# Kernel tuning notes

Measured on AMD Instinct MI355X. Metric: run time of the kernel, lower is better.

The kernel has to match this reference:

```python
import jax, jax.numpy as jnp
import numpy as np

D_K = 64

def setup_inputs() -> dict:
    key = jax.random.key(0)
    kx, kq, kk, kv = jax.random.split(key, 4)
    B, T, D = 4, 2048, 1024
    s = 1.0 / np.sqrt(D)
    return {
        "x": jax.random.normal(kx, (B, T, D), dtype=jnp.float32),
        "Wq": jax.random.normal(kq, (D, D_K), dtype=jnp.float32) * s,
        "Wk": jax.random.normal(kk, (D, D_K), dtype=jnp.float32) * s,
        "Wv": jax.random.normal(kv, (D, D_K), dtype=jnp.float32) * s,
    }

def reference(x, Wq, Wk, Wv):
    # x: [B, T, D]; Wq/Wk/Wv: [D, d_k]
    Q = x @ Wq  # [B, T, d_k]
    K = x @ Wk
    V = x @ Wv
    scale = 1.0 / jnp.sqrt(jnp.asarray(Q.shape[-1], Q.dtype))
    scores = jnp.einsum('btd,bsd->bts', Q, K) * scale  # [B, T, T]
    T = scores.shape[-1]
    causal = jnp.tril(jnp.ones((T, T), dtype=bool))  # keep lower-tri incl diag
    masked = jnp.where(causal, scores, -jnp.inf)
    attn = jax.nn.softmax(masked, axis=-1)  # dropout p=0.0 -> identity
    context = jnp.einsum('bts,bsd->btd', attn, V)  # [B, T, d_k]
    return context
```

## Files before the change

kernel.cpp:

```cpp
#include <hip/hip_runtime.h>
#include <math.h>

#define BT    8192
#define TSEQ  2048
#define DIN   1024
#define DK    64

typedef __attribute__((ext_vector_type(8))) short bf16x8;
typedef __attribute__((ext_vector_type(4))) short bf16x4;
typedef __attribute__((ext_vector_type(4))) float f32x4;

static __device__ inline unsigned short f2bf(float f) {
    union { float f; unsigned u; } v; v.f = f;
    unsigned r = v.u + 0x7fff + ((v.u >> 16) & 1);
    return (unsigned short)(r >> 16);
}

static __device__ inline bf16x4 cvt4(float4 a) {
    bf16x4 r;
    r[0] = (short)f2bf(a.x); r[1] = (short)f2bf(a.y);
    r[2] = (short)f2bf(a.z); r[3] = (short)f2bf(a.w);
    return r;
}

__global__ __launch_bounds__(256) void wt_kernel(
    const float* __restrict__ Wq, const float* __restrict__ Wk,
    const float* __restrict__ Wv, unsigned short* __restrict__ WT)
{
    __shared__ float ws[64][65];
    const int tid = threadIdx.x;
    const int mat = blockIdx.x >> 4;
    const int k0  = (blockIdx.x & 15) << 6;
    const float* W = (mat == 0) ? Wq : ((mat == 1) ? Wk : Wv);

    const int j = tid & 63;
    for (int i = tid >> 6; i < 64; i += 4)
        ws[i][j] = W[(size_t)(k0 + i) * DK + j];
    __syncthreads();

    const int n  = tid & 63;
    const int c0 = (tid >> 6) << 4;
    unsigned short* dst = WT + (size_t)(mat * 64 + n) * DIN + k0 + c0;
    #pragma unroll
    for (int c = 0; c < 16; ++c) dst[c] = f2bf(ws[c0 + c][n]);
}

__global__ __launch_bounds__(256, 2) void proj_kernel(
    const float* __restrict__ x, const unsigned short* __restrict__ WT,
    unsigned short* __restrict__ Qb, unsigned short* __restrict__ Kb,
    unsigned short* __restrict__ VT)
{
    __shared__ unsigned short xs[16][1032];
    __shared__ unsigned short wtb[192][72];
    const int tid = threadIdx.x;
    const int m0 = blockIdx.x * 16;

    {
        const int r = tid >> 4;
        const int c = (tid & 15) << 2;
        const float* src = x + (size_t)(m0 + r) * DIN + c;
        float4 tmp[16];
        #pragma unroll
        for (int s = 0; s < 16; ++s) tmp[s] = *(const float4*)(src + s * 64);
        #pragma unroll
        for (int s = 0; s < 16; ++s) *(bf16x4*)&xs[r][c + s * 64] = cvt4(tmp[s]);
    }

    const int lane = tid & 63;
    const int w    = tid >> 6;
    const int lr = lane & 15, lg = lane >> 4;

    f32x4 acc[3];
    #pragma unroll
    for (int nt = 0; nt < 3; ++nt) acc[nt] = (f32x4){0.f, 0.f, 0.f, 0.f};

    __syncthreads();

    for (int kc = 0; kc < 16; ++kc) {
        const int k0 = kc << 6;

        #pragma unroll
        for (int i = 0; i < 6; ++i) {
            const int c = tid + i * 256;
            const int n = c >> 3;
            const int sl = c & 7;
            *(bf16x8*)&wtb[n][((sl + n) & 7) << 3] =
                *(const bf16x8*)(WT + (size_t)n * DIN + k0 + (sl << 3));
        }
        __syncthreads();

        #pragma unroll
        for (int st = 0; st < 2; ++st) {
            const bf16x8 af = *(const bf16x8*)&xs[lr][k0 + (st << 5) + (lg << 3)];
            #pragma unroll
            for (int nt = 0; nt < 3; ++nt) {
                const int n = w * 48 + nt * 16 + lr;
                const int sl = (st << 2) + lg;
                const bf16x8 bf = *(const bf16x8*)&wtb[n][((sl + n) & 7) << 3];
                acc[nt] = __builtin_amdgcn_mfma_f32_16x16x32_bf16(af, bf, acc[nt], 0, 0, 0);
            }
        }
        __syncthreads();
    }

    const float qsc = 0.125f * 1.44269504088896340736f;
    #pragma unroll
    for (int nt = 0; nt < 3; ++nt) {
        const int gct = w * 3 + nt;
        #pragma unroll
        for (int r = 0; r < 4; ++r) {
            const int row = m0 + (lg << 2) + r;
            const float vv = acc[nt][r];
            if (gct < 4) {
                Qb[(size_t)row * DK + gct * 16 + lr] = f2bf(vv * qsc);
            } else if (gct < 8) {
                Kb[(size_t)row * DK + (gct - 4) * 16 + lr] = f2bf(vv);
            } else {
                const int d = (gct - 8) * 16 + lr;
                VT[((size_t)(row >> 11) * DK + d) * TSEQ + (row & (TSEQ - 1))] = f2bf(vv);
            }
        }
    }
}

__global__ __launch_bounds__(256, 2) void attn_kernel(
    const unsigned short* __restrict__ Qb, const unsigned short* __restrict__ Kb,
    const unsigned short* __restrict__ VT, float* __restrict__ O)
{
    __shared__ __align__(16) unsigned short P_lds[4][16][72];
    __shared__ float Opart[4][16][68];
    __shared__ float mpart[4][16];
    __shared__ float Lpart[4][16];

    const int lane = threadIdx.x & 63;
    const int w    = threadIdx.x >> 6;
    const int qt = ((blockIdx.x & 3) << 7) | (127 - (blockIdx.x >> 2));
    const int q0 = qt << 4;
    const int t0 = q0 & (TSEQ - 1);
    const int b  = q0 >> 11;
    const int lr = lane & 15;
    const int lg = lane >> 4;

    const unsigned short* Qrow = Qb + (size_t)(q0 + lr) * DK + (lg << 3);
    const bf16x8 qf0 = *(const bf16x8*)(Qrow);
    const bf16x8 qf1 = *(const bf16x8*)(Qrow + 32);

    const unsigned short* Kbase = Kb + (size_t)b * TSEQ * DK;
    const unsigned short* Vbase = VT + (size_t)b * DK * TSEQ;

    f32x4 oacc[4];
    #pragma unroll
    for (int dt = 0; dt < 4; ++dt) oacc[dt] = (f32x4){0.f, 0.f, 0.f, 0.f};
    float m[4] = {-INFINITY, -INFINITY, -INFINITY, -INFINITY};
    float L[4] = {0.f, 0.f, 0.f, 0.f};

    const int nkb = (t0 >> 6) + 1;

    bf16x8 kf0[4], kf1[4];
    if (w < nkb) {
        const int s0 = w << 6;
        #pragma unroll
        for (int ct = 0; ct < 4; ++ct) {
            const unsigned short* Krow =
                Kbase + (size_t)(s0 + ct * 16 + lr) * DK + (lg << 3);
            kf0[ct] = *(const bf16x8*)(Krow);
            kf1[ct] = *(const bf16x8*)(Krow + 32);
        }
    }

    for (int kb = w; kb < nkb; kb += 4) {
        const int s0 = kb << 6;

        f32x4 s[4];
        #pragma unroll
        for (int ct = 0; ct < 4; ++ct) {
            f32x4 a = (f32x4){0.f, 0.f, 0.f, 0.f};
            a = __builtin_amdgcn_mfma_f32_16x16x32_bf16(qf0, kf0[ct], a, 0, 0, 0);
            a = __builtin_amdgcn_mfma_f32_16x16x32_bf16(qf1, kf1[ct], a, 0, 0, 0);
            s[ct] = a;
        }

        bf16x8 vf0[4], vf1[4];
        #pragma unroll
        for (int dt = 0; dt < 4; ++dt) {
            const unsigned short* Vrow =
                Vbase + (size_t)(dt * 16 + lr) * TSEQ + s0 + (lg << 3);
            vf0[dt] = *(const bf16x8*)(Vrow);
            vf1[dt] = *(const bf16x8*)(Vrow + 32);
        }

        bf16x8 nk0[4], nk1[4];
        if (kb + 4 < nkb) {
            const int sn = (kb + 4) << 6;
            #pragma unroll
            for (int ct = 0; ct < 4; ++ct) {
                const unsigned short* Krow =
                    Kbase + (size_t)(sn + ct * 16 + lr) * DK + (lg << 3);
                nk0[ct] = *(const bf16x8*)(Krow);
                nk1[ct] = *(const bf16x8*)(Krow + 32);
            }
        }

        if (kb == nkb - 1) {
            #pragma unroll
            for (int ct = 0; ct < 4; ++ct)
                #pragma unroll
                for (int r = 0; r < 4; ++r)
                    if (s0 + ct * 16 + lr > t0 + lg * 4 + r) s[ct][r] = -INFINITY;
        }

        float pm[4];
        #pragma unroll
        for (int r = 0; r < 4; ++r)
            pm[r] = fmaxf(fmaxf(s[0][r], s[1][r]), fmaxf(s[2][r], s[3][r]));

        bool near = true;
        #pragma unroll
        for (int r = 0; r < 4; ++r)
            near = near && (pm[r] - m[r] <= 8.0f);

        if (!__all(near)) {
            float tmax[4];
            #pragma unroll
            for (int r = 0; r < 4; ++r) tmax[r] = pm[r];
            #pragma unroll
            for (int off = 1; off < 16; off <<= 1)
                #pragma unroll
                for (int r = 0; r < 4; ++r)
                    tmax[r] = fmaxf(tmax[r], __shfl_xor(tmax[r], off));

            float f[4];
            #pragma unroll
            for (int r = 0; r < 4; ++r) {
                const float mn = fmaxf(m[r], tmax[r]);
                f[r] = exp2f(m[r] - mn);
                m[r] = mn;
            }
            #pragma unroll
            for (int r = 0; r < 4; ++r) L[r] *= f[r];
            #pragma unroll
            for (int r = 0; r < 4; ++r) {
                oacc[0][r] *= f[r]; oacc[1][r] *= f[r];
                oacc[2][r] *= f[r]; oacc[3][r] *= f[r];
            }
        }

        float ps[4] = {0.f, 0.f, 0.f, 0.f};
        unsigned short pb[4][4];
        #pragma unroll
        for (int ct = 0; ct < 4; ++ct)
            #pragma unroll
            for (int r = 0; r < 4; ++r) {
                const float p = exp2f(s[ct][r] - m[r]);
                ps[r] += p;
                pb[ct][r] = f2bf(p);
            }
        #pragma unroll
        for (int r = 0; r < 4; ++r) L[r] += ps[r];

        #pragma unroll
        for (int ct = 0; ct < 4; ++ct)
            #pragma unroll
            for (int r = 0; r < 4; ++r)
                P_lds[w][lg * 4 + r][ct * 16 + lr] = pb[ct][r];
        asm volatile("s_waitcnt lgkmcnt(0)" ::: "memory");
        const bf16x8 pf0 = *(const bf16x8*)&P_lds[w][lr][(lg << 3)];
        const bf16x8 pf1 = *(const bf16x8*)&P_lds[w][lr][32 + (lg << 3)];

        #pragma unroll
        for (int dt = 0; dt < 4; ++dt) {
            oacc[dt] = __builtin_amdgcn_mfma_f32_16x16x32_bf16(pf0, vf0[dt], oacc[dt], 0, 0, 0);
            oacc[dt] = __builtin_amdgcn_mfma_f32_16x16x32_bf16(pf1, vf1[dt], oacc[dt], 0, 0, 0);
        }

        #pragma unroll
        for (int ct = 0; ct < 4; ++ct) { kf0[ct] = nk0[ct]; kf1[ct] = nk1[ct]; }
    }

    #pragma unroll
    for (int off = 1; off < 16; off <<= 1)
        #pragma unroll
        for (int r = 0; r < 4; ++r) L[r] += __shfl_xor(L[r], off);

    #pragma unroll
    for (int dt = 0; dt < 4; ++dt)
        #pragma unroll
        for (int r = 0; r < 4; ++r)
            Opart[w][(lg << 2) + r][dt * 16 + lr] = oacc[dt][r];
    if (lr == 0) {
        #pragma unroll
        for (int r = 0; r < 4; ++r) {
            mpart[w][(lg << 2) + r] = m[r];
            Lpart[w][(lg << 2) + r] = L[r];
        }
    }
    __syncthreads();

    #pragma unroll
    for (int r = 0; r < 4; ++r) {
        const int row = (lg << 2) + r;
        const float M = fmaxf(fmaxf(mpart[0][row], mpart[1][row]),
                              fmaxf(mpart[2][row], mpart[3][row]));
        float Lf = 0.f, o = 0.f;
        #pragma unroll
        for (int v = 0; v < 4; ++v) {
            const float fv = exp2f(mpart[v][row] - M);
            Lf += fv * Lpart[v][row];
            o  += fv * Opart[v][row][(w << 4) + lr];
        }
        O[(size_t)(q0 + row) * DK + (w << 4) + lr] = o / Lf;
    }
}

extern "C" void kernel_launch(void* const* d_in, const int* in_sizes, int n_in,
                              void* d_out, int out_size, void* d_ws, size_t ws_size,
                              hipStream_t stream) {
    const float* x  = (const float*)d_in[0];
    const float* Wq = (const float*)d_in[1];
    const float* Wk = (const float*)d_in[2];
    const float* Wv = (const float*)d_in[3];
    float* O = (float*)d_out;

    unsigned short* Qb = (unsigned short*)d_ws;
    unsigned short* Kb = Qb + (size_t)BT * DK;
    unsigned short* VT = Kb + (size_t)BT * DK;
    unsigned short* WT = VT + (size_t)BT * DK;

    wt_kernel  <<<dim3(48),  dim3(256), 0, stream>>>(Wq, Wk, Wv, WT);
    proj_kernel<<<dim3(512), dim3(256), 0, stream>>>(x, WT, Qb, Kb, VT);
    attn_kernel<<<dim3(512), dim3(256), 0, stream>>>(Qb, Kb, VT, O);
}
```

Baseline: 51.18 us.

## Register-prefetch per-wave weight tiles and drop block barriers in QKV projection

The projection kernel's weight staging changes so that each wave loads only its own 48 output columns into LDS, prefetching the next k-chunk into registers while computing on the current one. Because each wave now reads only the LDS rows it wrote, both per-iteration __syncthreads are replaced by an lgkmcnt wait. The V-transpose store also packs four consecutive rows into one 8-byte write. The risk is higher register pressure from the double-buffered fragments, and the correctness of the WAR reuse of LDS across iterations depends on per-wave ordering.

```diff
diff --git a/kernel.cpp b/kernel.cpp
--- a/kernel.cpp
+++ b/kernel.cpp
@@ -74,20 +74,40 @@
     #pragma unroll
     for (int nt = 0; nt < 3; ++nt) acc[nt] = (f32x4){0.f, 0.f, 0.f, 0.f};
 
+    const unsigned short* wt_w = WT + (size_t)w * 48 * DIN;
+    bf16x8 cur[6], nxt[6];
+    #pragma unroll
+    for (int i = 0; i < 6; ++i) {
+        const int c = lane + i * 64;
+        const int nl = c >> 3;
+        const int sl = c & 7;
+        cur[i] = *(const bf16x8*)(wt_w + (size_t)nl * DIN + (sl << 3));
+    }
+
     __syncthreads();
 
     for (int kc = 0; kc < 16; ++kc) {
         const int k0 = kc << 6;
 
+        if (kc + 1 < 16) {
+            #pragma unroll
+            for (int i = 0; i < 6; ++i) {
+                const int c = lane + i * 64;
+                const int nl = c >> 3;
+                const int sl = c & 7;
+                nxt[i] = *(const bf16x8*)(wt_w + (size_t)nl * DIN
+                                          + (k0 + 64) + (sl << 3));
+            }
+        }
+
         #pragma unroll
         for (int i = 0; i < 6; ++i) {
-            const int c = tid + i * 256;
-            const int n = c >> 3;
+            const int c = lane + i * 64;
+            const int n = w * 48 + (c >> 3);
             const int sl = c & 7;
-            *(bf16x8*)&wtb[n][((sl + n) & 7) << 3] =
-                *(const bf16x8*)(WT + (size_t)n * DIN + k0 + (sl << 3));
-        }
-        __syncthreads();
+            *(bf16x8*)&wtb[n][((sl + n) & 7) << 3] = cur[i];
+        }
+        asm volatile("s_waitcnt lgkmcnt(0)" ::: "memory");
 
         #pragma unroll
         for (int st = 0; st < 2; ++st) {
@@ -100,25 +120,32 @@
                 acc[nt] = __builtin_amdgcn_mfma_f32_16x16x32_bf16(af, bf, acc[nt], 0, 0, 0);
             }
         }
-        __syncthreads();
+
+        if (kc + 1 < 16) {
+            #pragma unroll
+            for (int i = 0; i < 6; ++i) cur[i] = nxt[i];
+        }
     }
 
     const float qsc = 0.125f * 1.44269504088896340736f;
     #pragma unroll
     for (int nt = 0; nt < 3; ++nt) {
         const int gct = w * 3 + nt;
-        #pragma unroll
-        for (int r = 0; r < 4; ++r) {
-            const int row = m0 + (lg << 2) + r;
-            const float vv = acc[nt][r];
-            if (gct < 4) {
-                Qb[(size_t)row * DK + gct * 16 + lr] = f2bf(vv * qsc);
-            } else if (gct < 8) {
-                Kb[(size_t)row * DK + (gct - 4) * 16 + lr] = f2bf(vv);
-            } else {
-                const int d = (gct - 8) * 16 + lr;
-                VT[((size_t)(row >> 11) * DK + d) * TSEQ + (row & (TSEQ - 1))] = f2bf(vv);
-            }
+        if (gct < 8) {
+            #pragma unroll
+            for (int r = 0; r < 4; ++r) {
+                const int row = m0 + (lg << 2) + r;
+                const float vv = acc[nt][r];
+                if (gct < 4) Qb[(size_t)row * DK + gct * 16 + lr] = f2bf(vv * qsc);
+                else         Kb[(size_t)row * DK + (gct - 4) * 16 + lr] = f2bf(vv);
+            }
+        } else {
+            const int d = (gct - 8) * 16 + lr;
+            const int t = m0 + (lg << 2);
+            ushort4 pk;
+            pk.x = f2bf(acc[nt][0]); pk.y = f2bf(acc[nt][1]);
+            pk.z = f2bf(acc[nt][2]); pk.w = f2bf(acc[nt][3]);
+            *(ushort4*)&VT[((size_t)(t >> 11) * DK + d) * TSEQ + (t & (TSEQ - 1))] = pk;
         }
     }
 }
```

After: 47.91 us. 6.4% less time.
